# Optimization experiments

Hardware: AMD Instinct MI355X
Metric: run time of the kernel (lower is better)

Reference implementation:

```python
import jax, jax.numpy as jnp
import numpy as np
from jax import lax

FLOOR = 1e-6

def setup_inputs() -> dict:
    key = jax.random.key(0)
    k1, = jax.random.split(key, 1)
    B, C, FREQ, T = 16, 2, 514, 4000  # FREQ = 2 * 257 (real/imag stacked)
    tf_rep = jax.random.normal(k1, (B, C, FREQ, T), dtype=jnp.float32)
    return {
        "tf_rep": tf_rep,
        "weights": jnp.full((1,), 0.04, dtype=jnp.float32),   # smooth (not per-channel)
        "alpha": jnp.full((C,), 0.96, dtype=jnp.float32),
        "delta": jnp.full((C,), 2.0, dtype=jnp.float32),
        "root": jnp.full((C,), 2.0, dtype=jnp.float32),
    }

def _ema(mag, weights):
    # mag: (B, C, F, T); weights: (1,) -> scalar-like broadcast
    w = jnp.clip(weights, 0.0, 1.0)
    xs = jnp.moveaxis(mag, -1, 0)  # (T, B, C, F)
    init = xs[0]                   # initial_state = mag[..., 0]
    def step(acc, x):
        acc = w * x + (1.0 - w) * acc
        return acc, acc
    _, ys = lax.scan(step, init, xs)
    return jnp.moveaxis(ys, 0, -1)  # (B, C, F, T)

def reference(tf_rep, weights, alpha, delta, root):
    # asteroid complex: real/imag halves stacked along dim=-2
    re, im = jnp.split(tf_rep, 2, axis=-2)
    mag = jnp.sqrt(re * re + im * im)          # (B, C, F, T)
    ema = _ema(mag, weights)
    a = jnp.minimum(alpha, 1.0)[None, :, None, None]
    one_over_root = (1.0 / jnp.maximum(root, 1.0))[None, :, None, None]
    d = delta[None, :, None, None]
    out = (mag / (FLOOR + ema) ** a + d) ** one_over_root - d ** one_over_root
    return out

if __name__ == "__main__":
    inp = setup_inputs()
    print(reference(**inp).shape)
```

## Files before the change

### kernel.cpp

```cpp
#include <hip/hip_runtime.h>

#define FLOOR_EPS 1e-6f

__device__ __forceinline__ float fast_exp2(float x) { return __builtin_amdgcn_exp2f(x); }
__device__ __forceinline__ float fast_log2(float x) { return __builtin_amdgcn_logf(x); }

__global__ __launch_bounds__(256) void pcen_kernel(
    const float* __restrict__ tf,
    const float* __restrict__ weights,
    const float* __restrict__ alpha,
    const float* __restrict__ delta,
    const float* __restrict__ root,
    float* __restrict__ out,
    int C, int F, int T)
{
    const int row  = blockIdx.x;
    const int bc   = row / F;
    const int c    = bc % C;
    const int tid  = threadIdx.x;
    const int lane = tid & 63;
    const int wv   = tid >> 6;

    float w = weights[0];
    w = fminf(fmaxf(w, 0.0f), 1.0f);
    const float q = 1.0f - w;

    const float a    = fminf(alpha[c], 1.0f);
    const float dl   = delta[c];
    const float oor  = 1.0f / fmaxf(root[c], 1.0f);
    const float door = fast_exp2(oor * fast_log2(dl));

    const long long re_off  = (long long)(row + bc * F) * T;
    const long long im_off  = re_off + (long long)F * T;
    const long long out_off = (long long)row * T;

    const int  t0     = tid * 16;
    const bool active = (t0 < T);

    float m[16];
    if (active) {
        const float4* rp = (const float4*)(tf + re_off + t0);
        const float4* ip = (const float4*)(tf + im_off + t0);
#pragma unroll
        for (int g = 0; g < 4; ++g) {
            float4 r4 = rp[g];
            float4 i4 = ip[g];
            m[4*g+0] = sqrtf(fmaf(r4.x, r4.x, i4.x * i4.x));
            m[4*g+1] = sqrtf(fmaf(r4.y, r4.y, i4.y * i4.y));
            m[4*g+2] = sqrtf(fmaf(r4.z, r4.z, i4.z * i4.z));
            m[4*g+3] = sqrtf(fmaf(r4.w, r4.w, i4.w * i4.w));
        }
    } else {
#pragma unroll
        for (int j = 0; j < 16; ++j) m[j] = 0.0f;
    }

    float p = (t0 == 0) ? m[0] : w * m[0];
#pragma unroll
    for (int j = 1; j < 16; ++j) p = fmaf(q, p, w * m[j]);

    const float q2    = q * q;
    const float q4    = q2 * q2;
    const float q8    = q4 * q4;
    const float q16   = q8 * q8;
    const float q32   = q16 * q16;
    const float q64   = q32 * q32;
    const float q128  = q64 * q64;
    const float q256  = q128 * q128;
    const float q512  = q256 * q256;
    const float q1024 = q512 * q512;

    float v = p;
    float o;
    o = __shfl_up(v, 1, 64);  if (lane >= 1)  v = fmaf(q16,  o, v);
    o = __shfl_up(v, 2, 64);  if (lane >= 2)  v = fmaf(q32,  o, v);
    o = __shfl_up(v, 4, 64);  if (lane >= 4)  v = fmaf(q64,  o, v);
    o = __shfl_up(v, 8, 64);  if (lane >= 8)  v = fmaf(q128, o, v);
    o = __shfl_up(v, 16, 64); if (lane >= 16) v = fmaf(q256, o, v);
    o = __shfl_up(v, 32, 64); if (lane >= 32) v = fmaf(q512, o, v);

    __shared__ float S[4];
    if (lane == 63) S[wv] = v;
    __syncthreads();

    float carry = 0.0f;
#pragma unroll
    for (int u = 0; u < 3; ++u)
        carry = (u < wv) ? fmaf(q1024, carry, S[u]) : carry;

    float e = __shfl_up(v, 1, 64);
    if (lane == 0) e = 0.0f;
    const float qlane = fast_exp2((float)(16 * lane) * fast_log2(q));
    const float cin   = fmaf(qlane, carry, e);

    const bool root_is_2 = (oor == 0.5f);
    float eacc = cin;
    float4* op = (float4*)(out + out_off + t0);
#pragma unroll
    for (int g = 0; g < 4; ++g) {
        float ov[4];
#pragma unroll
        for (int k = 0; k < 4; ++k) {
            const int j  = 4 * g + k;
            float bj = (t0 + j == 0) ? m[0] : w * m[j];
            eacc = fmaf(q, eacc, bj);
            float ratio = m[j] * fast_exp2(-a * fast_log2(FLOOR_EPS + eacc));
            float s = ratio + dl;
            float r = root_is_2 ? sqrtf(s) : fast_exp2(oor * fast_log2(s));
            ov[k] = r - door;
        }
        if (active) {
            op[g] = make_float4(ov[0], ov[1], ov[2], ov[3]);
        }
    }
}

extern "C" void kernel_launch(void* const* d_in, const int* in_sizes, int n_in,
                              void* d_out, int out_size, void* d_ws, size_t ws_size,
                              hipStream_t stream) {
    const float* tf      = (const float*)d_in[0];
    const float* weights = (const float*)d_in[1];
    const float* alpha   = (const float*)d_in[2];
    const float* delta   = (const float*)d_in[3];
    const float* root    = (const float*)d_in[4];
    float* out = (float*)d_out;

    const int B = 16, C = 2, F = 257, T = 4000;
    const int rows = B * C * F;

    pcen_kernel<<<dim3(rows), dim3(256), 0, stream>>>(
        tf, weights, alpha, delta, root, out, C, F, T);
}
```

Before: 400.5 us.

## Use 1024-thread blocks with 4 elements per thread for the EMA scan

Each row's 4000-step scan is now split across 1024 threads holding 4 timesteps each, instead of 256 threads holding 16. The shuffle scan powers and the cross-wave carry are adjusted to match, with 16 waves now combined through shared memory. The aim is more parallelism and fewer registers per thread for this memory-bound kernel. In exchange the serial carry loop over 15 waves is longer, the barrier spans larger blocks, and each thread issues smaller memory transactions.

```diff
diff --git a/kernel.cpp b/kernel.cpp
--- a/kernel.cpp
+++ b/kernel.cpp
@@ -5,7 +5,7 @@
 __device__ __forceinline__ float fast_exp2(float x) { return __builtin_amdgcn_exp2f(x); }
 __device__ __forceinline__ float fast_log2(float x) { return __builtin_amdgcn_logf(x); }
 
-__global__ __launch_bounds__(256) void pcen_kernel(
+__global__ __launch_bounds__(1024) void pcen_kernel(
     const float* __restrict__ tf,
     const float* __restrict__ weights,
     const float* __restrict__ alpha,
@@ -34,84 +34,71 @@
     const long long im_off  = re_off + (long long)F * T;
     const long long out_off = (long long)row * T;
 
-    const int  t0     = tid * 16;
+    const int  t0     = tid * 4;
     const bool active = (t0 < T);
 
-    float m[16];
+    float m[4];
     if (active) {
-        const float4* rp = (const float4*)(tf + re_off + t0);
-        const float4* ip = (const float4*)(tf + im_off + t0);
-#pragma unroll
-        for (int g = 0; g < 4; ++g) {
-            float4 r4 = rp[g];
-            float4 i4 = ip[g];
-            m[4*g+0] = sqrtf(fmaf(r4.x, r4.x, i4.x * i4.x));
-            m[4*g+1] = sqrtf(fmaf(r4.y, r4.y, i4.y * i4.y));
-            m[4*g+2] = sqrtf(fmaf(r4.z, r4.z, i4.z * i4.z));
-            m[4*g+3] = sqrtf(fmaf(r4.w, r4.w, i4.w * i4.w));
-        }
+        float4 r4 = *(const float4*)(tf + re_off + t0);
+        float4 i4 = *(const float4*)(tf + im_off + t0);
+        m[0] = sqrtf(fmaf(r4.x, r4.x, i4.x * i4.x));
+        m[1] = sqrtf(fmaf(r4.y, r4.y, i4.y * i4.y));
+        m[2] = sqrtf(fmaf(r4.z, r4.z, i4.z * i4.z));
+        m[3] = sqrtf(fmaf(r4.w, r4.w, i4.w * i4.w));
     } else {
-#pragma unroll
-        for (int j = 0; j < 16; ++j) m[j] = 0.0f;
+        m[0] = m[1] = m[2] = m[3] = 0.0f;
     }
 
     float p = (t0 == 0) ? m[0] : w * m[0];
 #pragma unroll
-    for (int j = 1; j < 16; ++j) p = fmaf(q, p, w * m[j]);
+    for (int j = 1; j < 4; ++j) p = fmaf(q, p, w * m[j]);
 
-    const float q2    = q * q;
-    const float q4    = q2 * q2;
-    const float q8    = q4 * q4;
-    const float q16   = q8 * q8;
-    const float q32   = q16 * q16;
-    const float q64   = q32 * q32;
-    const float q128  = q64 * q64;
-    const float q256  = q128 * q128;
-    const float q512  = q256 * q256;
-    const float q1024 = q512 * q512;
+    const float q2   = q * q;
+    const float q4   = q2 * q2;
+    const float q8   = q4 * q4;
+    const float q16  = q8 * q8;
+    const float q32  = q16 * q16;
+    const float q64  = q32 * q32;
+    const float q128 = q64 * q64;
+    const float q256 = q128 * q128;
 
     float v = p;
     float o;
-    o = __shfl_up(v, 1, 64);  if (lane >= 1)  v = fmaf(q16,  o, v);
-    o = __shfl_up(v, 2, 64);  if (lane >= 2)  v = fmaf(q32,  o, v);
-    o = __shfl_up(v, 4, 64);  if (lane >= 4)  v = fmaf(q64,  o, v);
-    o = __shfl_up(v, 8, 64);  if (lane >= 8)  v = fmaf(q128, o, v);
-    o = __shfl_up(v, 16, 64); if (lane >= 16) v = fmaf(q256, o, v);
-    o = __shfl_up(v, 32, 64); if (lane >= 32) v = fmaf(q512, o, v);
+    o = __shfl_up(v, 1, 64);  if (lane >= 1)  v = fmaf(q4,   o, v);
+    o = __shfl_up(v, 2, 64);  if (lane >= 2)  v = fmaf(q8,   o, v);
+    o = __shfl_up(v, 4, 64);  if (lane >= 4)  v = fmaf(q16,  o, v);
+    o = __shfl_up(v, 8, 64);  if (lane >= 8)  v = fmaf(q32,  o, v);
+    o = __shfl_up(v, 16, 64); if (lane >= 16) v = fmaf(q64,  o, v);
+    o = __shfl_up(v, 32, 64); if (lane >= 32) v = fmaf(q128, o, v);
 
-    __shared__ float S[4];
+    __shared__ float S[16];
     if (lane == 63) S[wv] = v;
     __syncthreads();
 
     float carry = 0.0f;
 #pragma unroll
-    for (int u = 0; u < 3; ++u)
-        carry = (u < wv) ? fmaf(q1024, carry, S[u]) : carry;
+    for (int u = 0; u < 15; ++u)
+        carry = (u < wv) ? fmaf(q256, carry, S[u]) : carry;
 
     float e = __shfl_up(v, 1, 64);
     if (lane == 0) e = 0.0f;
-    const float qlane = fast_exp2((float)(16 * lane) * fast_log2(q));
+    const float qlane = fast_exp2((float)(4 * lane) * fast_log2(q));
     const float cin   = fmaf(qlane, carry, e);
 
     const bool root_is_2 = (oor == 0.5f);
     float eacc = cin;
-    float4* op = (float4*)(out + out_off + t0);
+    float ov[4];
 #pragma unroll
-    for (int g = 0; g < 4; ++g) {
-        float ov[4];
-#pragma unroll
-        for (int k = 0; k < 4; ++k) {
-            const int j  = 4 * g + k;
-            float bj = (t0 + j == 0) ? m[0] : w * m[j];
-            eacc = fmaf(q, eacc, bj);
-            float ratio = m[j] * fast_exp2(-a * fast_log2(FLOOR_EPS + eacc));
-            float s = ratio + dl;
-            float r = root_is_2 ? sqrtf(s) : fast_exp2(oor * fast_log2(s));
-            ov[k] = r - door;
-        }
-        if (active) {
-            op[g] = make_float4(ov[0], ov[1], ov[2], ov[3]);
-        }
+    for (int j = 0; j < 4; ++j) {
+        float bj = (t0 + j == 0) ? m[0] : w * m[j];
+        eacc = fmaf(q, eacc, bj);
+        float ratio = m[j] * fast_exp2(-a * fast_log2(FLOOR_EPS + eacc));
+        float s = ratio + dl;
+        float r = root_is_2 ? sqrtf(s) : fast_exp2(oor * fast_log2(s));
+        ov[j] = r - door;
+    }
+    if (active) {
+        *(float4*)(out + out_off + t0) = make_float4(ov[0], ov[1], ov[2], ov[3]);
     }
 }
 
@@ -128,6 +115,6 @@
     const int B = 16, C = 2, F = 257, T = 4000;
     const int rows = B * C * F;
 
-    pcen_kernel<<<dim3(rows), dim3(256), 0, stream>>>(
+    pcen_kernel<<<dim3(rows), dim3(1024), 0, stream>>>(
         tf, weights, alpha, delta, root, out, C, F, T);
 }
```

After: 390.2 us. 2.6% less time.
